# Performance work log

Hardware: AMD Instinct MI355X
Metric: run time of the kernel (lower is better)

## Reference

```python
import jax, jax.numpy as jnp
import numpy as np

B, N, K, F_IN, F_OUT = 8, 2048, 32, 256, 256


def setup_inputs() -> dict:
    key = jax.random.key(0)
    ks = jax.random.split(key, 8)
    x = jax.random.normal(ks[0], (B, N, F_IN), dtype=jnp.float32)
    idx_neib = jax.random.randint(ks[1], (N, K), 0, N, dtype=jnp.int32)
    # Linear params (torch nn.Linear stores weight as [out, in])
    lim_x = np.sqrt(2.0) * np.sqrt(6.0 / (F_IN + F_OUT))  # xavier_uniform, gain=relu
    Wx_w = jax.random.uniform(ks[2], (F_OUT, F_IN), jnp.float32, -lim_x, lim_x)
    Wx_b = jnp.zeros((F_OUT,), jnp.float32)
    Wn_w = jax.random.uniform(ks[3], (F_OUT, F_IN), jnp.float32, -lim_x, lim_x)
    Wn_b = jnp.zeros((F_OUT,), jnp.float32)
    gamma = jnp.ones((2 * F_OUT,), jnp.float32)
    beta = jnp.zeros((2 * F_OUT,), jnp.float32)
    return {"x": x, "idx_neib": idx_neib, "Wx_w": Wx_w, "Wx_b": Wx_b,
            "Wn_w": Wn_w, "Wn_b": Wn_b, "gamma": gamma, "beta": beta}


def reference(x, idx_neib, Wx_w, Wx_b, Wn_w, Wn_b, gamma, beta):
    # Gather neighbor features: [B, N, K, F] then mean over the K neighbors.
    x_neib = jnp.take(x, idx_neib, axis=1).mean(axis=2)  # [B, N, F]
    # Dual linear projections (weights stored [out, in] as in torch).
    h_self = jnp.einsum('bnf,of->bno', x, Wx_w) + Wx_b
    h_nei = jnp.einsum('bnf,of->bno', x_neib, Wn_w) + Wn_b
    h = jnp.concatenate([h_self, h_nei], axis=2)          # [B, N, 2*out]
    # F.normalize(p=2, dim=2): divide by max(||h||_2, 1e-12)
    nrm = jnp.sqrt(jnp.sum(h * h, axis=2, keepdims=True))
    h = h / jnp.maximum(nrm, 1e-12)
    h = jax.nn.relu(h)
    # BatchNorm1d over channel dim (training mode: batch stats over B and N,
    # biased variance), eps=1e-5.
    mu = h.mean(axis=(0, 1))
    var = jnp.mean((h - mu) ** 2, axis=(0, 1))
    h = (h - mu) * jax.lax.rsqrt(var + 1e-5) * gamma + beta
    return h
```

## Files before the change

kernel.cpp:

```cpp
#include <hip/hip_runtime.h>
#include <stdint.h>

#define BB 8
#define NN 2048
#define KK 32
#define FIN 256
#define FOUT 256
#define CC 512
#define MM (BB*NN)
#define RB 32
#define NBLK (MM/RB)
#define LDA 264

typedef __attribute__((ext_vector_type(8))) short short8;
typedef __attribute__((ext_vector_type(4))) float f32x4;

__device__ __forceinline__ unsigned short f2bf(float f) {
    union { float f; unsigned u; } v; v.f = f;
    unsigned u = v.u;
    return (unsigned short)((u + 0x7FFFu + ((u >> 16) & 1u)) >> 16);
}
__device__ __forceinline__ float bf2f(unsigned short s) {
    union { unsigned u; float f; } v; v.u = ((unsigned)s) << 16;
    return v.f;
}

__global__ void k_pre(const float* __restrict__ x, const int* __restrict__ idx,
                      const float* __restrict__ Wx, const float* __restrict__ Wxb,
                      const float* __restrict__ Wn, const float* __restrict__ Wnb,
                      unsigned short* __restrict__ xb, unsigned short* __restrict__ xnb,
                      unsigned short* __restrict__ Wc, float* __restrict__ bc) {
    const int blk = blockIdx.x;
    const int tid = threadIdx.x;
    if (blk < 4096) {
        int b = blk & 7;
        int n = (blk >> 3) * 4 + (tid >> 6);
        int lane = tid & 63;
        const int* ip = idx + n * KK;
        const float* xbb = x + (size_t)b * NN * FIN + lane * 4;
        float a0 = 0.f, a1 = 0.f, a2 = 0.f, a3 = 0.f;
        #pragma unroll 8
        for (int k = 0; k < KK; ++k) {
            int j = ip[k];
            float4 v = *(const float4*)(xbb + (size_t)j * FIN);
            a0 += v.x; a1 += v.y; a2 += v.z; a3 += v.w;
        }
        const float s = 1.0f / (float)KK;
        ushort4 o; o.x = f2bf(a0 * s); o.y = f2bf(a1 * s); o.z = f2bf(a2 * s); o.w = f2bf(a3 * s);
        *(ushort4*)(xnb + ((size_t)b * NN + n) * FIN + lane * 4) = o;
    } else if (blk < 8192) {
        int c = blk - 4096;
        int b = c & 7, chunk = c >> 3;
        size_t f4 = (size_t)b * (NN * FIN / 4) + chunk * 256 + tid;
        float4 v = ((const float4*)x)[f4];
        ushort4 o; o.x = f2bf(v.x); o.y = f2bf(v.y); o.z = f2bf(v.z); o.w = f2bf(v.w);
        ((ushort4*)xb)[f4] = o;
    } else {
        int gid = (blk - 8192) * 256 + tid;
        int o = gid >> 8, k = gid & 255;
        float w = (o < FOUT) ? Wx[o * FIN + k] : Wn[(o - FOUT) * FIN + k];
        Wc[gid] = f2bf(w);
        if (gid < CC) bc[gid] = (gid < FOUT) ? Wxb[gid] : Wnb[gid - FOUT];
    }
}

__global__ __launch_bounds__(256, 2)
void k_gemm(const unsigned short* __restrict__ xb,
            const unsigned short* __restrict__ xnb,
            const unsigned short* __restrict__ Wc,
            const float* __restrict__ bc,
            unsigned short* __restrict__ h,
            float* __restrict__ psum, float* __restrict__ psq) {
    __shared__ unsigned short As[2][RB * LDA];
    __shared__ float sqpart[4][RB];
    __shared__ float rnorm[RB];

    const int tid  = threadIdx.x;
    const int w    = tid >> 6;
    const int lane = tid & 63;
    const int quad = lane >> 4;
    const int l16  = lane & 15;
    const int r0   = blockIdx.x * RB;

    {
        const uint4* gs = (const uint4*)(xb  + (size_t)r0 * FIN);
        const uint4* gn = (const uint4*)(xnb + (size_t)r0 * FIN);
        #pragma unroll
        for (int i = 0; i < 4; ++i) {
            int e = tid + i * 256;
            int row = e >> 5, col8 = e & 31;
            *(uint4*)&As[0][row * LDA + col8 * 8] = gs[e];
            *(uint4*)&As[1][row * LDA + col8 * 8] = gn[e];
        }
    }
    __syncthreads();

    const unsigned short* A = As[w >> 1];
    const int cb = w * 128;

    f32x4 acc[2][8];
    #pragma unroll
    for (int mt = 0; mt < 2; ++mt)
        #pragma unroll
        for (int nt = 0; nt < 8; ++nt) acc[mt][nt] = (f32x4){0.f, 0.f, 0.f, 0.f};

    const unsigned short* Bp = Wc + (size_t)(cb + l16) * FIN + quad * 8;
    const unsigned short* Ap = A + (size_t)l16 * LDA + quad * 8;

    #pragma unroll 2
    for (int k0 = 0; k0 < FIN; k0 += 32) {
        short8 a0 = *(const short8*)(Ap + k0);
        short8 a1 = *(const short8*)(Ap + 16 * LDA + k0);
        short8 bfr[8];
        #pragma unroll
        for (int nt = 0; nt < 8; ++nt)
            bfr[nt] = *(const short8*)(Bp + (size_t)nt * 16 * FIN + k0);
        #pragma unroll
        for (int nt = 0; nt < 8; ++nt) {
            acc[0][nt] = __builtin_amdgcn_mfma_f32_16x16x32_bf16(a0, bfr[nt], acc[0][nt], 0, 0, 0);
            acc[1][nt] = __builtin_amdgcn_mfma_f32_16x16x32_bf16(a1, bfr[nt], acc[1][nt], 0, 0, 0);
        }
    }

    float bcv[8];
    #pragma unroll
    for (int nt = 0; nt < 8; ++nt) bcv[nt] = bc[cb + nt * 16 + l16];

    float rsq[2][4] = {{0.f,0.f,0.f,0.f},{0.f,0.f,0.f,0.f}};
    #pragma unroll
    for (int mt = 0; mt < 2; ++mt)
        #pragma unroll
        for (int nt = 0; nt < 8; ++nt)
            #pragma unroll
            for (int r = 0; r < 4; ++r) {
                float v = acc[mt][nt][r] + bcv[nt];
                acc[mt][nt][r] = v;
                rsq[mt][r] += v * v;
            }
    #pragma unroll
    for (int off = 1; off < 16; off <<= 1)
        #pragma unroll
        for (int mt = 0; mt < 2; ++mt)
            #pragma unroll
            for (int r = 0; r < 4; ++r)
                rsq[mt][r] += __shfl_xor(rsq[mt][r], off, 64);
    if (l16 == 0) {
        #pragma unroll
        for (int mt = 0; mt < 2; ++mt)
            #pragma unroll
            for (int r = 0; r < 4; ++r)
                sqpart[w][mt * 16 + quad * 4 + r] = rsq[mt][r];
    }
    __syncthreads();
    if (tid < RB) {
        float tot = sqpart[0][tid] + sqpart[1][tid] + sqpart[2][tid] + sqpart[3][tid];
        rnorm[tid] = 1.0f / fmaxf(sqrtf(tot), 1e-12f);
    }
    __syncthreads();

    float csum[8] = {0.f,0.f,0.f,0.f,0.f,0.f,0.f,0.f};
    float csq [8] = {0.f,0.f,0.f,0.f,0.f,0.f,0.f,0.f};
    #pragma unroll
    for (int mt = 0; mt < 2; ++mt) {
        #pragma unroll
        for (int r = 0; r < 4; ++r) {
            int row = mt * 16 + quad * 4 + r;
            float rn = rnorm[row];
            unsigned short* hp = h + (size_t)(r0 + row) * CC + cb + l16;
            #pragma unroll
            for (int nt = 0; nt < 8; ++nt) {
                float v = fmaxf(acc[mt][nt][r] * rn, 0.0f);
                hp[nt * 16] = f2bf(v);
                csum[nt] += v;
                csq [nt] += v * v;
            }
        }
    }
    #pragma unroll
    for (int off = 16; off < 64; off <<= 1)
        #pragma unroll
        for (int nt = 0; nt < 8; ++nt) {
            csum[nt] += __shfl_xor(csum[nt], off, 64);
            csq [nt] += __shfl_xor(csq [nt], off, 64);
        }
    if (quad == 0) {
        #pragma unroll
        for (int nt = 0; nt < 8; ++nt) {
            int c = cb + nt * 16 + l16;
            psum[(size_t)c * NBLK + blockIdx.x] = csum[nt];
            psq [(size_t)c * NBLK + blockIdx.x] = csq [nt];
        }
    }
}

__global__ void k_stats(const float* __restrict__ psum, const float* __restrict__ psq,
                        const float* __restrict__ gamma, const float* __restrict__ beta,
                        float* __restrict__ ss) {
    __shared__ float ps[4], pq[4];
    int c = blockIdx.x, t = threadIdx.x;
    float s = psum[(size_t)c * NBLK + t] + psum[(size_t)c * NBLK + 256 + t];
    float q = psq [(size_t)c * NBLK + t] + psq [(size_t)c * NBLK + 256 + t];
    #pragma unroll
    for (int off = 32; off; off >>= 1) { s += __shfl_xor(s, off, 64); q += __shfl_xor(q, off, 64); }
    int w = t >> 6, lane = t & 63;
    if (lane == 0) { ps[w] = s; pq[w] = q; }
    __syncthreads();
    if (t == 0) {
        float S = ps[0] + ps[1] + ps[2] + ps[3];
        float Q = pq[0] + pq[1] + pq[2] + pq[3];
        const float inv = 1.0f / (float)MM;
        float mu  = S * inv;
        float var = fmaxf(Q * inv - mu * mu, 0.0f);
        float sc  = gamma[c] * rsqrtf(var + 1e-5f);
        ss[c]      = sc;
        ss[CC + c] = beta[c] - mu * sc;
    }
}

__global__ void k_apply(const unsigned short* __restrict__ h,
                        const float* __restrict__ ss,
                        float* __restrict__ out) {
    int gid = blockIdx.x * 256 + threadIdx.x;
    int c0 = (gid * 4) & (CC - 1);
    ushort4 hv = ((const ushort4*)h)[gid];
    float4 sc = *(const float4*)(ss + c0);
    float4 sh = *(const float4*)(ss + CC + c0);
    float4 o;
    o.x = bf2f(hv.x) * sc.x + sh.x;
    o.y = bf2f(hv.y) * sc.y + sh.y;
    o.z = bf2f(hv.z) * sc.z + sh.z;
    o.w = bf2f(hv.w) * sc.w + sh.w;
    ((float4*)out)[gid] = o;
}

extern "C" void kernel_launch(void* const* d_in, const int* in_sizes, int n_in,
                              void* d_out, int out_size, void* d_ws, size_t ws_size,
                              hipStream_t stream) {
    const float* x     = (const float*)d_in[0];
    const int*   idx   = (const int*)  d_in[1];
    const float* Wx_w  = (const float*)d_in[2];
    const float* Wx_b  = (const float*)d_in[3];
    const float* Wn_w  = (const float*)d_in[4];
    const float* Wn_b  = (const float*)d_in[5];
    const float* gamma = (const float*)d_in[6];
    const float* beta  = (const float*)d_in[7];
    float* out = (float*)d_out;

    char* p = (char*)d_ws;
    unsigned short* xb  = (unsigned short*)p; p += (size_t)MM * FIN * 2;
    unsigned short* xnb = (unsigned short*)p; p += (size_t)MM * FIN * 2;
    unsigned short* Wc  = (unsigned short*)p; p += (size_t)CC * FIN * 2;
    float* bc           = (float*)p;          p += (size_t)CC * 4;
    unsigned short* h   = (unsigned short*)p; p += (size_t)MM * CC * 2;
    float* psum         = (float*)p;          p += (size_t)CC * NBLK * 4;
    float* psq          = (float*)p;          p += (size_t)CC * NBLK * 4;
    float* ss           = (float*)p;          p += (size_t)2 * CC * 4;

    hipLaunchKernelGGL(k_pre,   dim3(8704), dim3(256), 0, stream,
                       x, idx, Wx_w, Wx_b, Wn_w, Wn_b, xb, xnb, Wc, bc);
    hipLaunchKernelGGL(k_gemm,  dim3(NBLK), dim3(256), 0, stream, xb, xnb, Wc, bc, h, psum, psq);
    hipLaunchKernelGGL(k_stats, dim3(CC),   dim3(256), 0, stream, psum, psq, gamma, beta, ss);
    hipLaunchKernelGGL(k_apply, dim3(8192), dim3(256), 0, stream, h, ss, out);
}
```

Before: 141.9 us.

## Fuse all stages into one cooperative kernel with grid-wide syncs

Replaces the four-kernel pipeline (pre-conversion, GEMM, stats, apply) with a single cooperative kernel. Each block gathers its neighbour means and converts its x rows straight into shared memory, then syncs the grid, runs the GEMM, and publishes partial column sums. After a further grid sync it reduces the BN statistics and, after a third, applies them to accumulators held in registers. This removes the global round trips for the bf16 x, x_neib and h intermediates plus three launch gaps, at the cost of three grid barriers and requiring all 512 blocks to be co-resident.

```diff
diff --git a/kernel.cpp b/kernel.cpp
--- a/kernel.cpp
+++ b/kernel.cpp
@@ -1,4 +1,5 @@
 #include <hip/hip_runtime.h>
+#include <hip/hip_cooperative_groups.h>
 #include <stdint.h>
 
 #define BB 8
@@ -20,80 +21,70 @@
     unsigned u = v.u;
     return (unsigned short)((u + 0x7FFFu + ((u >> 16) & 1u)) >> 16);
 }
-__device__ __forceinline__ float bf2f(unsigned short s) {
-    union { unsigned u; float f; } v; v.u = ((unsigned)s) << 16;
-    return v.f;
-}
-
-__global__ void k_pre(const float* __restrict__ x, const int* __restrict__ idx,
-                      const float* __restrict__ Wx, const float* __restrict__ Wxb,
-                      const float* __restrict__ Wn, const float* __restrict__ Wnb,
-                      unsigned short* __restrict__ xb, unsigned short* __restrict__ xnb,
-                      unsigned short* __restrict__ Wc, float* __restrict__ bc) {
-    const int blk = blockIdx.x;
-    const int tid = threadIdx.x;
-    if (blk < 4096) {
-        int b = blk & 7;
-        int n = (blk >> 3) * 4 + (tid >> 6);
-        int lane = tid & 63;
-        const int* ip = idx + n * KK;
-        const float* xbb = x + (size_t)b * NN * FIN + lane * 4;
-        float a0 = 0.f, a1 = 0.f, a2 = 0.f, a3 = 0.f;
-        #pragma unroll 8
-        for (int k = 0; k < KK; ++k) {
-            int j = ip[k];
-            float4 v = *(const float4*)(xbb + (size_t)j * FIN);
-            a0 += v.x; a1 += v.y; a2 += v.z; a3 += v.w;
-        }
-        const float s = 1.0f / (float)KK;
-        ushort4 o; o.x = f2bf(a0 * s); o.y = f2bf(a1 * s); o.z = f2bf(a2 * s); o.w = f2bf(a3 * s);
-        *(ushort4*)(xnb + ((size_t)b * NN + n) * FIN + lane * 4) = o;
-    } else if (blk < 8192) {
-        int c = blk - 4096;
-        int b = c & 7, chunk = c >> 3;
-        size_t f4 = (size_t)b * (NN * FIN / 4) + chunk * 256 + tid;
-        float4 v = ((const float4*)x)[f4];
-        ushort4 o; o.x = f2bf(v.x); o.y = f2bf(v.y); o.z = f2bf(v.z); o.w = f2bf(v.w);
-        ((ushort4*)xb)[f4] = o;
-    } else {
-        int gid = (blk - 8192) * 256 + tid;
-        int o = gid >> 8, k = gid & 255;
-        float w = (o < FOUT) ? Wx[o * FIN + k] : Wn[(o - FOUT) * FIN + k];
-        Wc[gid] = f2bf(w);
-        if (gid < CC) bc[gid] = (gid < FOUT) ? Wxb[gid] : Wnb[gid - FOUT];
-    }
-}
 
 __global__ __launch_bounds__(256, 2)
-void k_gemm(const unsigned short* __restrict__ xb,
-            const unsigned short* __restrict__ xnb,
-            const unsigned short* __restrict__ Wc,
-            const float* __restrict__ bc,
-            unsigned short* __restrict__ h,
-            float* __restrict__ psum, float* __restrict__ psq) {
+void k_fused(const float* __restrict__ x, const int* __restrict__ idx,
+             const float* __restrict__ Wx, const float* __restrict__ Wxb,
+             const float* __restrict__ Wn, const float* __restrict__ Wnb,
+             const float* __restrict__ gamma, const float* __restrict__ beta,
+             unsigned short* __restrict__ Wc, float* __restrict__ bc,
+             float* __restrict__ psum, float* __restrict__ psq,
+             float* __restrict__ ss, float* __restrict__ out) {
+    namespace cg = cooperative_groups;
+    cg::grid_group grid = cg::this_grid();
+
     __shared__ unsigned short As[2][RB * LDA];
     __shared__ float sqpart[4][RB];
     __shared__ float rnorm[RB];
-
+    __shared__ float red[8];
+
+    const int bid  = blockIdx.x;
     const int tid  = threadIdx.x;
     const int w    = tid >> 6;
     const int lane = tid & 63;
     const int quad = lane >> 4;
     const int l16  = lane & 15;
-    const int r0   = blockIdx.x * RB;
-
-    {
-        const uint4* gs = (const uint4*)(xb  + (size_t)r0 * FIN);
-        const uint4* gn = (const uint4*)(xnb + (size_t)r0 * FIN);
-        #pragma unroll
-        for (int i = 0; i < 4; ++i) {
+    const int b    = bid & 7;
+    const int n0   = (bid >> 3) * RB;
+    const float* xbat = x + (size_t)b * NN * FIN;
+
+    {
+        int gid = bid * 256 + tid;
+        int o = gid >> 8, k = gid & 255;
+        float wv = (o < FOUT) ? Wx[o * FIN + k] : Wn[(o - FOUT) * FIN + k];
+        Wc[gid] = f2bf(wv);
+        if (gid < CC) bc[gid] = (gid < FOUT) ? Wxb[gid] : Wnb[gid - FOUT];
+    }
+    {
+        const float4* gs = (const float4*)(xbat + (size_t)n0 * FIN);
+        #pragma unroll
+        for (int i = 0; i < 8; ++i) {
             int e = tid + i * 256;
-            int row = e >> 5, col8 = e & 31;
-            *(uint4*)&As[0][row * LDA + col8 * 8] = gs[e];
-            *(uint4*)&As[1][row * LDA + col8 * 8] = gn[e];
-        }
-    }
-    __syncthreads();
+            float4 v = gs[e];
+            ushort4 o4; o4.x = f2bf(v.x); o4.y = f2bf(v.y); o4.z = f2bf(v.z); o4.w = f2bf(v.w);
+            *(ushort4*)&As[0][(e >> 6) * LDA + (e & 63) * 4] = o4;
+        }
+    }
+    {
+        #pragma unroll
+        for (int rr = 0; rr < 8; ++rr) {
+            int n = n0 + w * 8 + rr;
+            const int* ip = idx + n * KK;
+            const float* xp = xbat + lane * 4;
+            float a0 = 0.f, a1 = 0.f, a2 = 0.f, a3 = 0.f;
+            #pragma unroll 8
+            for (int k = 0; k < KK; ++k) {
+                float4 v = *(const float4*)(xp + (size_t)ip[k] * FIN);
+                a0 += v.x; a1 += v.y; a2 += v.z; a3 += v.w;
+            }
+            const float s = 1.0f / (float)KK;
+            ushort4 o4; o4.x = f2bf(a0 * s); o4.y = f2bf(a1 * s);
+            o4.z = f2bf(a2 * s); o4.w = f2bf(a3 * s);
+            *(ushort4*)&As[1][(w * 8 + rr) * LDA + lane * 4] = o4;
+        }
+    }
+    __threadfence();
+    grid.sync();
 
     const unsigned short* A = As[w >> 1];
     const int cb = w * 128;
@@ -161,21 +152,18 @@
     float csum[8] = {0.f,0.f,0.f,0.f,0.f,0.f,0.f,0.f};
     float csq [8] = {0.f,0.f,0.f,0.f,0.f,0.f,0.f,0.f};
     #pragma unroll
-    for (int mt = 0; mt < 2; ++mt) {
+    for (int mt = 0; mt < 2; ++mt)
         #pragma unroll
         for (int r = 0; r < 4; ++r) {
-            int row = mt * 16 + quad * 4 + r;
-            float rn = rnorm[row];
-            unsigned short* hp = h + (size_t)(r0 + row) * CC + cb + l16;
+            float rn = rnorm[mt * 16 + quad * 4 + r];
             #pragma unroll
             for (int nt = 0; nt < 8; ++nt) {
                 float v = fmaxf(acc[mt][nt][r] * rn, 0.0f);
-                hp[nt * 16] = f2bf(v);
+                acc[mt][nt][r] = v;
                 csum[nt] += v;
                 csq [nt] += v * v;
             }
         }
-    }
     #pragma unroll
     for (int off = 16; off < 64; off <<= 1)
         #pragma unroll
@@ -187,50 +175,55 @@
         #pragma unroll
         for (int nt = 0; nt < 8; ++nt) {
             int c = cb + nt * 16 + l16;
-            psum[(size_t)c * NBLK + blockIdx.x] = csum[nt];
-            psq [(size_t)c * NBLK + blockIdx.x] = csq [nt];
-        }
-    }
-}
-
-__global__ void k_stats(const float* __restrict__ psum, const float* __restrict__ psq,
-                        const float* __restrict__ gamma, const float* __restrict__ beta,
-                        float* __restrict__ ss) {
-    __shared__ float ps[4], pq[4];
-    int c = blockIdx.x, t = threadIdx.x;
-    float s = psum[(size_t)c * NBLK + t] + psum[(size_t)c * NBLK + 256 + t];
-    float q = psq [(size_t)c * NBLK + t] + psq [(size_t)c * NBLK + 256 + t];
-    #pragma unroll
-    for (int off = 32; off; off >>= 1) { s += __shfl_xor(s, off, 64); q += __shfl_xor(q, off, 64); }
-    int w = t >> 6, lane = t & 63;
-    if (lane == 0) { ps[w] = s; pq[w] = q; }
-    __syncthreads();
-    if (t == 0) {
-        float S = ps[0] + ps[1] + ps[2] + ps[3];
-        float Q = pq[0] + pq[1] + pq[2] + pq[3];
-        const float inv = 1.0f / (float)MM;
-        float mu  = S * inv;
-        float var = fmaxf(Q * inv - mu * mu, 0.0f);
-        float sc  = gamma[c] * rsqrtf(var + 1e-5f);
-        ss[c]      = sc;
-        ss[CC + c] = beta[c] - mu * sc;
-    }
-}
-
-__global__ void k_apply(const unsigned short* __restrict__ h,
-                        const float* __restrict__ ss,
-                        float* __restrict__ out) {
-    int gid = blockIdx.x * 256 + threadIdx.x;
-    int c0 = (gid * 4) & (CC - 1);
-    ushort4 hv = ((const ushort4*)h)[gid];
-    float4 sc = *(const float4*)(ss + c0);
-    float4 sh = *(const float4*)(ss + CC + c0);
-    float4 o;
-    o.x = bf2f(hv.x) * sc.x + sh.x;
-    o.y = bf2f(hv.y) * sc.y + sh.y;
-    o.z = bf2f(hv.z) * sc.z + sh.z;
-    o.w = bf2f(hv.w) * sc.w + sh.w;
-    ((float4*)out)[gid] = o;
+            psum[(size_t)c * NBLK + bid] = csum[nt];
+            psq [(size_t)c * NBLK + bid] = csq [nt];
+        }
+    }
+    __threadfence();
+    grid.sync();
+
+    {
+        int c = bid;
+        float s = psum[(size_t)c * NBLK + tid] + psum[(size_t)c * NBLK + 256 + tid];
+        float q = psq [(size_t)c * NBLK + tid] + psq [(size_t)c * NBLK + 256 + tid];
+        #pragma unroll
+        for (int off = 32; off; off >>= 1) {
+            s += __shfl_xor(s, off, 64);
+            q += __shfl_xor(q, off, 64);
+        }
+        if (lane == 0) { red[w] = s; red[4 + w] = q; }
+        __syncthreads();
+        if (tid == 0) {
+            float S = red[0] + red[1] + red[2] + red[3];
+            float Q = red[4] + red[5] + red[6] + red[7];
+            const float inv = 1.0f / (float)MM;
+            float mu  = S * inv;
+            float var = fmaxf(Q * inv - mu * mu, 0.0f);
+            float sc  = gamma[c] * rsqrtf(var + 1e-5f);
+            ss[c]      = sc;
+            ss[CC + c] = beta[c] - mu * sc;
+        }
+    }
+    __threadfence();
+    grid.sync();
+
+    float sc[8], sh[8];
+    #pragma unroll
+    for (int nt = 0; nt < 8; ++nt) {
+        int c = cb + nt * 16 + l16;
+        sc[nt] = ss[c];
+        sh[nt] = ss[CC + c];
+    }
+    #pragma unroll
+    for (int mt = 0; mt < 2; ++mt)
+        #pragma unroll
+        for (int r = 0; r < 4; ++r) {
+            int row = mt * 16 + quad * 4 + r;
+            float* op = out + ((size_t)b * NN + n0 + row) * CC + cb + l16;
+            #pragma unroll
+            for (int nt = 0; nt < 8; ++nt)
+                op[nt * 16] = acc[mt][nt][r] * sc[nt] + sh[nt];
+        }
 }
 
 extern "C" void kernel_launch(void* const* d_in, const int* in_sizes, int n_in,
@@ -247,18 +240,17 @@
     float* out = (float*)d_out;
 
     char* p = (char*)d_ws;
-    unsigned short* xb  = (unsigned short*)p; p += (size_t)MM * FIN * 2;
-    unsigned short* xnb = (unsigned short*)p; p += (size_t)MM * FIN * 2;
-    unsigned short* Wc  = (unsigned short*)p; p += (size_t)CC * FIN * 2;
-    float* bc           = (float*)p;          p += (size_t)CC * 4;
-    unsigned short* h   = (unsigned short*)p; p += (size_t)MM * CC * 2;
-    float* psum         = (float*)p;          p += (size_t)CC * NBLK * 4;
-    float* psq          = (float*)p;          p += (size_t)CC * NBLK * 4;
-    float* ss           = (float*)p;          p += (size_t)2 * CC * 4;
-
-    hipLaunchKernelGGL(k_pre,   dim3(8704), dim3(256), 0, stream,
-                       x, idx, Wx_w, Wx_b, Wn_w, Wn_b, xb, xnb, Wc, bc);
-    hipLaunchKernelGGL(k_gemm,  dim3(NBLK), dim3(256), 0, stream, xb, xnb, Wc, bc, h, psum, psq);
-    hipLaunchKernelGGL(k_stats, dim3(CC),   dim3(256), 0, stream, psum, psq, gamma, beta, ss);
-    hipLaunchKernelGGL(k_apply, dim3(8192), dim3(256), 0, stream, h, ss, out);
+    unsigned short* Wc = (unsigned short*)p; p += (size_t)CC * FIN * 2;
+    float* bc          = (float*)p;          p += (size_t)CC * 4;
+    float* psum        = (float*)p;          p += (size_t)CC * NBLK * 4;
+    float* psq         = (float*)p;          p += (size_t)CC * NBLK * 4;
+    float* ss          = (float*)p;          p += (size_t)2 * CC * 4;
+
+    void* args[] = {
+        (void*)&x, (void*)&idx, (void*)&Wx_w, (void*)&Wx_b, (void*)&Wn_w, (void*)&Wn_b,
+        (void*)&gamma, (void*)&beta, (void*)&Wc, (void*)&bc,
+        (void*)&psum, (void*)&psq, (void*)&ss, (void*)&out
+    };
+    hipLaunchCooperativeKernel((const void*)k_fused, dim3(NBLK), dim3(256),
+                               args, 0, stream);
 }
```

After: 462.4 us. 3.26x slower.

## Fuse x-to-bf16 conversion into GEMM tile load and widen apply vectors

Applied to the files above, without the earlier changes.

Removes the separate pass that converts x to a bf16 buffer. The GEMM kernel now reads fp32 x directly and converts it while staging into shared memory, which saves a full write and re-read of the bf16 copy. The GEMM launch bounds are raised to 3 blocks per CU, and the apply kernel processes 8 elements per thread instead of 4. The GEMM staging now reads twice the bytes for the self half and adds conversion work before the first sync, and the higher occupancy target may force register spills.

```diff
diff --git a/kernel.cpp b/kernel.cpp
--- a/kernel.cpp
+++ b/kernel.cpp
@@ -28,44 +28,38 @@
 __global__ void k_pre(const float* __restrict__ x, const int* __restrict__ idx,
                       const float* __restrict__ Wx, const float* __restrict__ Wxb,
                       const float* __restrict__ Wn, const float* __restrict__ Wnb,
-                      unsigned short* __restrict__ xb, unsigned short* __restrict__ xnb,
+                      unsigned short* __restrict__ xnb,
                       unsigned short* __restrict__ Wc, float* __restrict__ bc) {
     const int blk = blockIdx.x;
     const int tid = threadIdx.x;
-    if (blk < 4096) {
-        int b = blk & 7;
-        int n = (blk >> 3) * 4 + (tid >> 6);
-        int lane = tid & 63;
-        const int* ip = idx + n * KK;
-        const float* xbb = x + (size_t)b * NN * FIN + lane * 4;
-        float a0 = 0.f, a1 = 0.f, a2 = 0.f, a3 = 0.f;
-        #pragma unroll 8
-        for (int k = 0; k < KK; ++k) {
-            int j = ip[k];
-            float4 v = *(const float4*)(xbb + (size_t)j * FIN);
-            a0 += v.x; a1 += v.y; a2 += v.z; a3 += v.w;
-        }
-        const float s = 1.0f / (float)KK;
-        ushort4 o; o.x = f2bf(a0 * s); o.y = f2bf(a1 * s); o.z = f2bf(a2 * s); o.w = f2bf(a3 * s);
-        *(ushort4*)(xnb + ((size_t)b * NN + n) * FIN + lane * 4) = o;
-    } else if (blk < 8192) {
-        int c = blk - 4096;
-        int b = c & 7, chunk = c >> 3;
-        size_t f4 = (size_t)b * (NN * FIN / 4) + chunk * 256 + tid;
-        float4 v = ((const float4*)x)[f4];
-        ushort4 o; o.x = f2bf(v.x); o.y = f2bf(v.y); o.z = f2bf(v.z); o.w = f2bf(v.w);
-        ((ushort4*)xb)[f4] = o;
-    } else {
-        int gid = (blk - 8192) * 256 + tid;
+    if (blk < 512) {
+        int gid = blk * 256 + tid;
         int o = gid >> 8, k = gid & 255;
         float w = (o < FOUT) ? Wx[o * FIN + k] : Wn[(o - FOUT) * FIN + k];
         Wc[gid] = f2bf(w);
         if (gid < CC) bc[gid] = (gid < FOUT) ? Wxb[gid] : Wnb[gid - FOUT];
-    }
-}
-
-__global__ __launch_bounds__(256, 2)
-void k_gemm(const unsigned short* __restrict__ xb,
+    } else {
+        int g = blk - 512;
+        int b = g & 7;
+        int n = (g >> 3) * 4 + (tid >> 6);
+        int lane = tid & 63;
+        const int* ip = idx + n * KK;
+        const float* xp = x + (size_t)b * NN * FIN + lane * 4;
+        float a0 = 0.f, a1 = 0.f, a2 = 0.f, a3 = 0.f;
+        #pragma unroll 8
+        for (int k = 0; k < KK; ++k) {
+            float4 v = *(const float4*)(xp + (size_t)ip[k] * FIN);
+            a0 += v.x; a1 += v.y; a2 += v.z; a3 += v.w;
+        }
+        const float s = 1.0f / (float)KK;
+        ushort4 o4; o4.x = f2bf(a0 * s); o4.y = f2bf(a1 * s);
+        o4.z = f2bf(a2 * s); o4.w = f2bf(a3 * s);
+        *(ushort4*)(xnb + ((size_t)b * NN + n) * FIN + lane * 4) = o4;
+    }
+}
+
+__global__ __launch_bounds__(256, 3)
+void k_gemm(const float* __restrict__ x,
             const unsigned short* __restrict__ xnb,
             const unsigned short* __restrict__ Wc,
             const float* __restrict__ bc,
@@ -83,14 +77,21 @@
     const int r0   = blockIdx.x * RB;
 
     {
-        const uint4* gs = (const uint4*)(xb  + (size_t)r0 * FIN);
+        const float4* gs = (const float4*)(x + (size_t)r0 * FIN);
+        #pragma unroll
+        for (int i = 0; i < 8; ++i) {
+            int e = tid + i * 256;
+            float4 v = gs[e];
+            ushort4 o4; o4.x = f2bf(v.x); o4.y = f2bf(v.y); o4.z = f2bf(v.z); o4.w = f2bf(v.w);
+            *(ushort4*)&As[0][(e >> 6) * LDA + (e & 63) * 4] = o4;
+        }
+    }
+    {
         const uint4* gn = (const uint4*)(xnb + (size_t)r0 * FIN);
         #pragma unroll
         for (int i = 0; i < 4; ++i) {
             int e = tid + i * 256;
-            int row = e >> 5, col8 = e & 31;
-            *(uint4*)&As[0][row * LDA + col8 * 8] = gs[e];
-            *(uint4*)&As[1][row * LDA + col8 * 8] = gn[e];
+            *(uint4*)&As[1][(e >> 5) * LDA + (e & 31) * 8] = gn[e];
         }
     }
     __syncthreads();
@@ -221,16 +222,24 @@
                         const float* __restrict__ ss,
                         float* __restrict__ out) {
     int gid = blockIdx.x * 256 + threadIdx.x;
-    int c0 = (gid * 4) & (CC - 1);
-    ushort4 hv = ((const ushort4*)h)[gid];
-    float4 sc = *(const float4*)(ss + c0);
-    float4 sh = *(const float4*)(ss + CC + c0);
-    float4 o;
-    o.x = bf2f(hv.x) * sc.x + sh.x;
-    o.y = bf2f(hv.y) * sc.y + sh.y;
-    o.z = bf2f(hv.z) * sc.z + sh.z;
-    o.w = bf2f(hv.w) * sc.w + sh.w;
-    ((float4*)out)[gid] = o;
+    int c0 = (gid * 8) & (CC - 1);
+    uint4 hv = ((const uint4*)h)[gid];
+    const unsigned short* hs = (const unsigned short*)&hv;
+    float4 sc0 = *(const float4*)(ss + c0);
+    float4 sc1 = *(const float4*)(ss + c0 + 4);
+    float4 sh0 = *(const float4*)(ss + CC + c0);
+    float4 sh1 = *(const float4*)(ss + CC + c0 + 4);
+    float4 o0, o1;
+    o0.x = bf2f(hs[0]) * sc0.x + sh0.x;
+    o0.y = bf2f(hs[1]) * sc0.y + sh0.y;
+    o0.z = bf2f(hs[2]) * sc0.z + sh0.z;
+    o0.w = bf2f(hs[3]) * sc0.w + sh0.w;
+    o1.x = bf2f(hs[4]) * sc1.x + sh1.x;
+    o1.y = bf2f(hs[5]) * sc1.y + sh1.y;
+    o1.z = bf2f(hs[6]) * sc1.z + sh1.z;
+    o1.w = bf2f(hs[7]) * sc1.w + sh1.w;
+    ((float4*)out)[gid * 2]     = o0;
+    ((float4*)out)[gid * 2 + 1] = o1;
 }
 
 extern "C" void kernel_launch(void* const* d_in, const int* in_sizes, int n_in,
@@ -247,7 +256,6 @@
     float* out = (float*)d_out;
 
     char* p = (char*)d_ws;
-    unsigned short* xb  = (unsigned short*)p; p += (size_t)MM * FIN * 2;
     unsigned short* xnb = (unsigned short*)p; p += (size_t)MM * FIN * 2;
     unsigned short* Wc  = (unsigned short*)p; p += (size_t)CC * FIN * 2;
     float* bc           = (float*)p;          p += (size_t)CC * 4;
@@ -256,9 +264,9 @@
     float* psq          = (float*)p;          p += (size_t)CC * NBLK * 4;
     float* ss           = (float*)p;          p += (size_t)2 * CC * 4;
 
-    hipLaunchKernelGGL(k_pre,   dim3(8704), dim3(256), 0, stream,
-                       x, idx, Wx_w, Wx_b, Wn_w, Wn_b, xb, xnb, Wc, bc);
-    hipLaunchKernelGGL(k_gemm,  dim3(NBLK), dim3(256), 0, stream, xb, xnb, Wc, bc, h, psum, psq);
+    hipLaunchKernelGGL(k_pre,   dim3(4608), dim3(256), 0, stream,
+                       x, idx, Wx_w, Wx_b, Wn_w, Wn_b, xnb, Wc, bc);
+    hipLaunchKernelGGL(k_gemm,  dim3(NBLK), dim3(256), 0, stream, x, xnb, Wc, bc, h, psum, psq);
     hipLaunchKernelGGL(k_stats, dim3(CC),   dim3(256), 0, stream, psum, psq, gamma, beta, ss);
-    hipLaunchKernelGGL(k_apply, dim3(8192), dim3(256), 0, stream, h, ss, out);
-}
+    hipLaunchKernelGGL(k_apply, dim3(4096), dim3(256), 0, stream, h, ss, out);
+}
```

After: 139.2 us. No clear change (-1.9%).
